# Optimization experiments

Measured on AMD Instinct MI355X. Metric: run time of the kernel, lower is better.

Reference implementation:

```python
import jax, jax.numpy as jnp
import numpy as np

D_MODEL = 1024
N_HEADS = 16
D_HEAD = D_MODEL // N_HEADS
B, S = 2, 2048


def setup_inputs() -> dict:
    key = jax.random.key(0)
    ks = jax.random.split(key, 8)
    scale = 1.0 / np.sqrt(D_MODEL)
    return {
        "x": jax.random.normal(ks[0], (B, S, D_MODEL), dtype=jnp.float32),
        "Wq": jax.random.normal(ks[1], (D_MODEL, D_MODEL), dtype=jnp.float32) * scale,
        "bq": jnp.zeros((D_MODEL,), dtype=jnp.float32),
        "Wk": jax.random.normal(ks[2], (D_MODEL, D_MODEL), dtype=jnp.float32) * scale,
        "bk": jnp.zeros((D_MODEL,), dtype=jnp.float32),
        "Wv": jax.random.normal(ks[3], (D_MODEL, D_MODEL), dtype=jnp.float32) * scale,
        "bv": jnp.zeros((D_MODEL,), dtype=jnp.float32),
        "Wo": jax.random.normal(ks[4], (D_MODEL, D_MODEL), dtype=jnp.float32) * scale,
    }


def reference(x, Wq, bq, Wk, bk, Wv, bv, Wo):
    Bsz, Slen, D = x.shape
    # projections -> [B, H, S, Dh]
    def split_heads(t):
        return t.reshape(Bsz, Slen, N_HEADS, D_HEAD).transpose(0, 2, 1, 3)
    q = split_heads(x @ Wq + bq)
    k = split_heads(x @ Wk + bk)
    v = split_heads(x @ Wv + bv)
    scale = jnp.sqrt(jnp.float32(D_HEAD))
    scores = jnp.einsum('bhsd,bhtd->bhst', q, k) / scale  # [B,H,S,S]
    causal_mask = jnp.tril(jnp.ones((Slen, Slen), dtype=jnp.bool_))
    scores = jnp.where(causal_mask, scores, jnp.finfo(scores.dtype).min)
    attn = jax.nn.softmax(scores, axis=-1)
    # deterministic=True path: dropout is identity
    out = jnp.einsum('bhst,bhtd->bhsd', attn, v)
    out = out.transpose(0, 2, 1, 3).reshape(Bsz, Slen, D)
    return out @ Wo
```

## Files before the change

### kernel.cpp

```cpp
#include <hip/hip_runtime.h>
#include <hip/hip_bf16.h>

#define BATCH   2
#define SEQ     2048
#define DMODEL  1024
#define NHEADS  16
#define DHEAD   64
#define MROWS   (BATCH*SEQ)

typedef float  f32x4  __attribute__((ext_vector_type(4)));
typedef short  s16x4  __attribute__((ext_vector_type(4)));
typedef short  s16x8  __attribute__((ext_vector_type(8)));
typedef __bf16 bf16x8 __attribute__((ext_vector_type(8)));

__device__ __forceinline__ short f2bf(float f) {
  union { float f; unsigned u; } v; v.f = f;
  return (short)((v.u + 0x7fffu + ((v.u >> 16) & 1u)) >> 16);
}

__global__ void convert_x(const float* __restrict__ x, short* __restrict__ xb) {
  int i = (blockIdx.x * 256 + threadIdx.x) * 4;
  float4 v = *(const float4*)(x + i);
  s16x4 o = { f2bf(v.x), f2bf(v.y), f2bf(v.z), f2bf(v.w) };
  *(s16x4*)(xb + i) = o;
}

__global__ void transpose_w(const float* __restrict__ Wq, const float* __restrict__ Wk,
                            const float* __restrict__ Wv, const float* __restrict__ Wo,
                            short* __restrict__ WtQKV, short* __restrict__ WtO) {
  __shared__ float t[32][33];
  const float* W; short* Wt;
  int z = blockIdx.z;
  if      (z == 0) { W = Wq; Wt = WtQKV; }
  else if (z == 1) { W = Wk; Wt = WtQKV + (1u << 20); }
  else if (z == 2) { W = Wv; Wt = WtQKV + (2u << 20); }
  else             { W = Wo; Wt = WtO; }
  int n0 = blockIdx.x * 32, k0 = blockIdx.y * 32;
  int tx = threadIdx.x, ty = threadIdx.y;
  #pragma unroll
  for (int i = 0; i < 32; i += 8) t[ty + i][tx] = W[(k0 + ty + i) * DMODEL + n0 + tx];
  __syncthreads();
  #pragma unroll
  for (int i = 0; i < 32; i += 8) Wt[(n0 + ty + i) * DMODEL + k0 + tx] = f2bf(t[tx][ty + i]);
}

template<int MT, int NT, int EPI>
__global__ __launch_bounds__(256) void gemm_bf16(
    const short* __restrict__ A, const short* __restrict__ Bt,
    const float* __restrict__ bq, const float* __restrict__ bk, const float* __restrict__ bv,
    short* __restrict__ qb, short* __restrict__ kb, short* __restrict__ vt,
    float* __restrict__ out)
{
  constexpr int K = DMODEL, BK = 32;
  constexpr int WM = MT / 2, WN = NT / 2;
  constexpr int TM = WM / 16, TN = WN / 16;
  constexpr int CA = MT * BK / 512;
  constexpr int CB = NT * BK / 512;
  constexpr int TP = 136;
  constexpr int SME = (EPI == 0) ? 128 * TP : (MT * BK + NT * BK);
  __shared__ short smem[SME];
  short* la = smem;
  short* lb = smem + MT * BK;
  const int tid = threadIdx.x;
  const int wave = tid >> 6, lane = tid & 63;
  const int quad = lane >> 4, l16 = lane & 15;
  const int wr = wave >> 1, wc = wave & 1;
  const int m0 = blockIdx.y * MT, n0 = blockIdx.x * NT;
  const int arow = lane >> 2, acol = (lane & 3) * 8;

  f32x4 acc[TM][TN] = {};

  for (int k0 = 0; k0 < K; k0 += BK) {
    for (int c = wave; c < CA; c += 4) {
      const short* gp = A + (m0 + c * 16 + arow) * K + k0 + acol;
      __builtin_amdgcn_global_load_lds((__attribute__((address_space(1))) void*)gp,
                                       (__attribute__((address_space(3))) void*)(la + c * 512),
                                       16, 0, 0);
    }
    for (int c = wave; c < CB; c += 4) {
      const short* gp = Bt + (n0 + c * 16 + arow) * K + k0 + acol;
      __builtin_amdgcn_global_load_lds((__attribute__((address_space(1))) void*)gp,
                                       (__attribute__((address_space(3))) void*)(lb + c * 512),
                                       16, 0, 0);
    }
    __syncthreads();
    bf16x8 af[TM], bfr[TN];
    #pragma unroll
    for (int i = 0; i < TM; ++i)
      af[i] = *(const bf16x8*)&la[(wr * WM + i * 16 + l16) * BK + quad * 8];
    #pragma unroll
    for (int j = 0; j < TN; ++j)
      bfr[j] = *(const bf16x8*)&lb[(wc * WN + j * 16 + l16) * BK + quad * 8];
    #pragma unroll
    for (int i = 0; i < TM; ++i)
      #pragma unroll
      for (int j = 0; j < TN; ++j)
        acc[i][j] = __builtin_amdgcn_mfma_f32_16x16x32_bf16(af[i], bfr[j], acc[i][j], 0, 0, 0);
    __syncthreads();
  }

  if constexpr (EPI == 0) {
    const bool isV = (n0 >= 2 * DMODEL);
    const float* bias; int nbase; float scl;
    if (n0 < DMODEL)          { bias = bq; nbase = 0;          scl = 0.125f * 1.44269504089f; }
    else if (n0 < 2 * DMODEL) { bias = bk; nbase = DMODEL;     scl = 1.f; }
    else                      { bias = bv; nbase = 2 * DMODEL; scl = 1.f; }
    #pragma unroll
    for (int j = 0; j < TN; ++j) {
      int coll = wc * WN + j * 16 + l16;
      float bias_v = bias[n0 - nbase + coll];
      #pragma unroll
      for (int i = 0; i < TM; ++i) {
        int rowl = wr * WM + i * 16 + quad * 4;
        #pragma unroll
        for (int r = 0; r < 4; ++r) {
          short v = f2bf((acc[i][j][r] + bias_v) * scl);
          if (isV) smem[coll * TP + rowl + r] = v;
          else     smem[(rowl + r) * TP + coll] = v;
        }
      }
    }
    __syncthreads();
    const int b = m0 >> 11, s0 = m0 & (SEQ - 1);
    const int rseg = tid & 15, rrow = tid >> 4;
    if (!isV) {
      short* dst = (n0 < DMODEL) ? qb : kb;
      #pragma unroll
      for (int it = 0; it < 8; ++it) {
        int row = it * 16 + rrow;
        int colg = (n0 - nbase) + rseg * 8;
        int h = colg >> 6, d = colg & 63;
        s16x8 v = *(const s16x8*)&smem[row * TP + rseg * 8];
        *(s16x8*)(dst + ((b * NHEADS + h) * SEQ + s0 + row) * DHEAD + d) = v;
      }
    } else {
      #pragma unroll
      for (int it = 0; it < 8; ++it) {
        int drow = it * 16 + rrow;
        int colg = (n0 - nbase) + drow;
        int h = colg >> 6, d = colg & 63;
        s16x8 v = *(const s16x8*)&smem[drow * TP + rseg * 8];
        *(s16x8*)(vt + ((b * NHEADS + h) * DHEAD + d) * SEQ + s0 + rseg * 8) = v;
      }
    }
  } else {
    #pragma unroll
    for (int i = 0; i < TM; ++i)
      #pragma unroll
      for (int r = 0; r < 4; ++r) {
        int mrow = m0 + wr * WM + i * 16 + quad * 4 + r;
        #pragma unroll
        for (int j = 0; j < TN; ++j)
          out[mrow * DMODEL + n0 + wc * WN + j * 16 + l16] = acc[i][j][r];
      }
    (void)bq; (void)bk; (void)bv; (void)qb; (void)kb; (void)vt;
  }
}


__global__ __launch_bounds__(128, 2) void attn_k(
    const short* __restrict__ qbp, const short* __restrict__ kbp,
    const short* __restrict__ vtb, short* __restrict__ ob)
{
  __shared__ short kls[2][4096];
  __shared__ short vls[2][4096];
  const int tid = threadIdx.x, wave = tid >> 6, lane = tid & 63;
  const int quad = lane >> 4, l16 = lane & 15;
  const int bh = blockIdx.x >> 5;
  const int qg = blockIdx.x & 31;
  const int qt = qg * 2 + wave;
  const int ma = qt * 16;
  const int mb = (127 - qt) * 16;
  const int nch = (127 - qg * 2) / 4 + 1;
  const short* Q  = qbp + bh * SEQ * DHEAD;
  const short* Kp = kbp + bh * SEQ * DHEAD;
  const short* Vt = vtb + bh * DHEAD * SEQ;

  bf16x8 qa0 = *(const bf16x8*)&Q[(ma + l16) * DHEAD + quad * 8];
  bf16x8 qa1 = *(const bf16x8*)&Q[(ma + l16) * DHEAD + 32 + quad * 8];
  bf16x8 qb0 = *(const bf16x8*)&Q[(mb + l16) * DHEAD + quad * 8];
  bf16x8 qb1 = *(const bf16x8*)&Q[(mb + l16) * DHEAD + 32 + quad * 8];

  float lA = 0.f, lB = 0.f;
  f32x4 oA[4] = {}, oB[4] = {};

  const int vdl = lane >> 3, vsl = lane & 7;

  auto stage = [&](int buf, int t0) {
    #pragma unroll
    for (int j = 0; j < 4; ++j) {
      int g = j * 2 + wave;
      const short* gp = Kp + (t0 + lane) * DHEAD + g * 8;
      __builtin_amdgcn_global_load_lds((__attribute__((address_space(1))) void*)gp,
                                       (__attribute__((address_space(3))) void*)&kls[buf][g * 512],
                                       16, 0, 0);
    }
    #pragma unroll
    for (int j = 0; j < 4; ++j) {
      int gd = j * 2 + wave;
      const short* gp = Vt + (gd * 8 + vdl) * SEQ + t0 + ((vsl ^ vdl) * 8);
      __builtin_amdgcn_global_load_lds((__attribute__((address_space(1))) void*)gp,
                                       (__attribute__((address_space(3))) void*)&vls[buf][gd * 512],
                                       16, 0, 0);
    }
  };

  auto frag = [&](const bf16x8 kf[4][2], const s16x4 vf[4][4], int t0, int mF,
                  bf16x8 f0, bf16x8 f1, float& lF, f32x4 oF[4]) {
    const int nlive = (mF - t0) / 16 + 1;
    #pragma unroll
    for (int t = 0; t < 4; ++t) {
      if (t < nlive) {
        f32x4 a = {};
        a = __builtin_amdgcn_mfma_f32_16x16x32_bf16(kf[t][0], f0, a, 0, 0, 0);
        a = __builtin_amdgcn_mfma_f32_16x16x32_bf16(kf[t][1], f1, a, 0, 0, 0);
        if (t0 + t * 16 == mF) {
          #pragma unroll
          for (int r = 0; r < 4; ++r)
            if (quad * 4 + r > l16) a[r] = -1e30f;
        }
        f32x4 p;
        #pragma unroll
        for (int r = 0; r < 4; ++r) p[r] = __builtin_amdgcn_exp2f(a[r]);
        lF += (p[0] + p[1]) + (p[2] + p[3]);
        __hip_bfloat162 c01 = __float22bfloat162_rn(float2{p[0], p[1]});
        __hip_bfloat162 c23 = __float22bfloat162_rn(float2{p[2], p[3]});
        union { unsigned u[2]; s16x4 s; } pu;
        pu.u[0] = *(unsigned*)&c01; pu.u[1] = *(unsigned*)&c23;
        #pragma unroll
        for (int dt = 0; dt < 4; ++dt)
          oF[dt] = __builtin_amdgcn_mfma_f32_16x16x16bf16_1k(pu.s, vf[t][dt], oF[dt], 0, 0, 0);
      }
    }
  };

  stage(0, 0);
  for (int c = 0; c < nch; ++c) {
    __syncthreads();
    if (c + 1 < nch) stage((c + 1) & 1, (c + 1) * 64);
    const int t0 = c * 64;
    const int buf = c & 1;
    bf16x8 kf[4][2];
    #pragma unroll
    for (int t = 0; t < 4; ++t)
      #pragma unroll
      for (int h = 0; h < 2; ++h)
        kf[t][h] = *(const bf16x8*)&kls[buf][((h * 4 + quad) * 64 + t * 16 + l16) * 8];
    s16x4 vf[4][4];
    #pragma unroll
    for (int t = 0; t < 4; ++t) {
      int gsw = ((t * 2 + (quad >> 1)) ^ (l16 & 7));
      #pragma unroll
      for (int dt = 0; dt < 4; ++dt)
        vf[t][dt] = *(const s16x4*)&vls[buf][((dt * 16 + l16) * 8 + gsw) * 8 + (quad & 1) * 4];
    }
    if (t0 <= mb) frag(kf, vf, t0, mb, qb0, qb1, lB, oB);
    if (t0 <= ma) frag(kf, vf, t0, ma, qa0, qa1, lA, oA);
  }

  lA += __shfl_xor(lA, 16, 64); lA += __shfl_xor(lA, 32, 64);
  lB += __shfl_xor(lB, 16, 64); lB += __shfl_xor(lB, 32, 64);
  const int b = bh >> 4, h = bh & 15;
  #pragma unroll
  for (int r = 0; r < 4; ++r) {
    float liA = 1.0f / __shfl(lA, quad * 4 + r, 64);
    float liB = 1.0f / __shfl(lB, quad * 4 + r, 64);
    int sA = ma + quad * 4 + r, sB = mb + quad * 4 + r;
    #pragma unroll
    for (int dt = 0; dt < 4; ++dt) {
      ob[(b * SEQ + sA) * DMODEL + h * DHEAD + dt * 16 + l16] = f2bf(oA[dt][r] * liA);
      ob[(b * SEQ + sB) * DMODEL + h * DHEAD + dt * 16 + l16] = f2bf(oB[dt][r] * liB);
    }
  }
}

extern "C" void kernel_launch(void* const* d_in, const int* in_sizes, int n_in,
                              void* d_out, int out_size, void* d_ws, size_t ws_size,
                              hipStream_t stream) {
  const float* x  = (const float*)d_in[0];
  const float* Wq = (const float*)d_in[1];
  const float* bq = (const float*)d_in[2];
  const float* Wk = (const float*)d_in[3];
  const float* bk = (const float*)d_in[4];
  const float* Wv = (const float*)d_in[5];
  const float* bv = (const float*)d_in[6];
  const float* Wo = (const float*)d_in[7];
  float* out = (float*)d_out;

  char* ws = (char*)d_ws;
  short* xb  = (short*)(ws);
  short* wtq = (short*)(ws + (8u  << 20));
  short* wto = (short*)(ws + (14u << 20));
  short* qb  = (short*)(ws + (16u << 20));
  short* kb  = (short*)(ws + (24u << 20));
  short* vt  = (short*)(ws + (32u << 20));
  short* ob  = (short*)(ws + (40u << 20));

  convert_x<<<MROWS * DMODEL / 1024, 256, 0, stream>>>(x, xb);
  transpose_w<<<dim3(32, 32, 4), dim3(32, 8), 0, stream>>>(Wq, Wk, Wv, Wo, wtq, wto);

  gemm_bf16<128, 128, 0><<<dim3(3 * DMODEL / 128, MROWS / 128), 256, 0, stream>>>(
      xb, wtq, bq, bk, bv, qb, kb, vt, nullptr);

  attn_k<<<BATCH * NHEADS * 32, 128, 0, stream>>>(qb, kb, vt, ob);

  gemm_bf16<64, 128, 1><<<dim3(DMODEL / 128, MROWS / 64), 256, 0, stream>>>(
      ob, wto, nullptr, nullptr, nullptr, nullptr, nullptr, nullptr, out);
}
```

Before: 207.0 us.

## Split attention KV range across two blocks and merge partial outputs

The attention kernel now uses 4 waves per block, each block covering 4 query tiles paired causally. Each block processes only alternating 64-key chunks (even or odd by a half index), so the KV loop is split across two blocks. Unnormalized partial outputs and row sums go to workspace, and a new merge kernel adds them and normalizes. This aims to cut per-block serial loop length and balance work, at the cost of extra partial-output traffic, an extra launch, and bf16 rounding of the partials before the merge.

```diff
diff --git a/kernel.cpp b/kernel.cpp
--- a/kernel.cpp
+++ b/kernel.cpp
@@ -7,6 +7,7 @@
 #define NHEADS  16
 #define DHEAD   64
 #define MROWS   (BATCH*SEQ)
+#define NBH     (BATCH*NHEADS)
 
 typedef float  f32x4  __attribute__((ext_vector_type(4)));
 typedef short  s16x4  __attribute__((ext_vector_type(4)));
@@ -16,6 +17,10 @@
 __device__ __forceinline__ short f2bf(float f) {
   union { float f; unsigned u; } v; v.f = f;
   return (short)((v.u + 0x7fffu + ((v.u >> 16) & 1u)) >> 16);
+}
+__device__ __forceinline__ float bf2f(short s) {
+  union { unsigned u; float f; } v; v.u = ((unsigned)(unsigned short)s) << 16;
+  return v.f;
 }
 
 __global__ void convert_x(const float* __restrict__ x, short* __restrict__ xb) {
@@ -158,20 +163,21 @@
 }
 
 
-__global__ __launch_bounds__(128, 2) void attn_k(
+__global__ __launch_bounds__(256, 2) void attn_k(
     const short* __restrict__ qbp, const short* __restrict__ kbp,
-    const short* __restrict__ vtb, short* __restrict__ ob)
+    const short* __restrict__ vtb, short* __restrict__ oP, float* __restrict__ lP)
 {
   __shared__ short kls[2][4096];
   __shared__ short vls[2][4096];
   const int tid = threadIdx.x, wave = tid >> 6, lane = tid & 63;
   const int quad = lane >> 4, l16 = lane & 15;
-  const int bh = blockIdx.x >> 5;
-  const int qg = blockIdx.x & 31;
-  const int qt = qg * 2 + wave;
+  const int half = blockIdx.x & 1;
+  const int bh = (blockIdx.x >> 1) & 31;
+  const int qg = blockIdx.x >> 6;
+  const int qt = qg * 4 + wave;
   const int ma = qt * 16;
   const int mb = (127 - qt) * 16;
-  const int nch = (127 - qg * 2) / 4 + 1;
+  const int nch = (127 - qg * 4) / 4 + 1;
   const short* Q  = qbp + bh * SEQ * DHEAD;
   const short* Kp = kbp + bh * SEQ * DHEAD;
   const short* Vt = vtb + bh * DHEAD * SEQ;
@@ -188,16 +194,16 @@
 
   auto stage = [&](int buf, int t0) {
     #pragma unroll
-    for (int j = 0; j < 4; ++j) {
-      int g = j * 2 + wave;
+    for (int j = 0; j < 2; ++j) {
+      int g = j * 4 + wave;
       const short* gp = Kp + (t0 + lane) * DHEAD + g * 8;
       __builtin_amdgcn_global_load_lds((__attribute__((address_space(1))) void*)gp,
                                        (__attribute__((address_space(3))) void*)&kls[buf][g * 512],
                                        16, 0, 0);
     }
     #pragma unroll
-    for (int j = 0; j < 4; ++j) {
-      int gd = j * 2 + wave;
+    for (int j = 0; j < 2; ++j) {
+      int gd = j * 4 + wave;
       const short* gp = Vt + (gd * 8 + vdl) * SEQ + t0 + ((vsl ^ vdl) * 8);
       __builtin_amdgcn_global_load_lds((__attribute__((address_space(1))) void*)gp,
                                        (__attribute__((address_space(3))) void*)&vls[buf][gd * 512],
@@ -234,12 +240,12 @@
     }
   };
 
-  stage(0, 0);
-  for (int c = 0; c < nch; ++c) {
+  stage(0, half * 64);
+  for (int c = half; c < nch; c += 2) {
     __syncthreads();
-    if (c + 1 < nch) stage((c + 1) & 1, (c + 1) * 64);
+    if (c + 2 < nch) stage(((c >> 1) + 1) & 1, (c + 2) * 64);
     const int t0 = c * 64;
-    const int buf = c & 1;
+    const int buf = (c >> 1) & 1;
     bf16x8 kf[4][2];
     #pragma unroll
     for (int t = 0; t < 4; ++t)
@@ -260,18 +266,32 @@
 
   lA += __shfl_xor(lA, 16, 64); lA += __shfl_xor(lA, 32, 64);
   lB += __shfl_xor(lB, 16, 64); lB += __shfl_xor(lB, 32, 64);
-  const int b = bh >> 4, h = bh & 15;
+  float* lD = lP + (half * NBH + bh) * SEQ;
+  if (quad == 0) { lD[ma + l16] = lA; lD[mb + l16] = lB; }
+  short* oD = oP + ((half * NBH + bh) * SEQ) * DHEAD;
   #pragma unroll
   for (int r = 0; r < 4; ++r) {
-    float liA = 1.0f / __shfl(lA, quad * 4 + r, 64);
-    float liB = 1.0f / __shfl(lB, quad * 4 + r, 64);
     int sA = ma + quad * 4 + r, sB = mb + quad * 4 + r;
     #pragma unroll
     for (int dt = 0; dt < 4; ++dt) {
-      ob[(b * SEQ + sA) * DMODEL + h * DHEAD + dt * 16 + l16] = f2bf(oA[dt][r] * liA);
-      ob[(b * SEQ + sB) * DMODEL + h * DHEAD + dt * 16 + l16] = f2bf(oB[dt][r] * liB);
+      oD[sA * DHEAD + dt * 16 + l16] = f2bf(oA[dt][r]);
+      oD[sB * DHEAD + dt * 16 + l16] = f2bf(oB[dt][r]);
     }
   }
+}
+
+__global__ void attn_merge(const short* __restrict__ oP, const float* __restrict__ lP,
+                           short* __restrict__ ob) {
+  int idx = blockIdx.x * 256 + threadIdx.x;
+  int d8 = idx & 7, s = (idx >> 3) & (SEQ - 1), bh = idx >> 14;
+  s16x8 e = *(const s16x8*)&oP[((0   + bh) * SEQ + s) * DHEAD + d8 * 8];
+  s16x8 o = *(const s16x8*)&oP[((NBH + bh) * SEQ + s) * DHEAD + d8 * 8];
+  float linv = 1.0f / (lP[bh * SEQ + s] + lP[(NBH + bh) * SEQ + s]);
+  s16x8 r;
+  #pragma unroll
+  for (int k = 0; k < 8; ++k) r[k] = f2bf((bf2f(e[k]) + bf2f(o[k])) * linv);
+  int b = bh >> 4, h = bh & 15;
+  *(s16x8*)&ob[(b * SEQ + s) * DMODEL + h * DHEAD + d8 * 8] = r;
 }
 
 extern "C" void kernel_launch(void* const* d_in, const int* in_sizes, int n_in,
@@ -290,11 +310,13 @@
   char* ws = (char*)d_ws;
   short* xb  = (short*)(ws);
   short* wtq = (short*)(ws + (8u  << 20));
-  short* wto = (short*)(ws + (14u << 20));
+  short* oP  = (short*)(ws);
   short* qb  = (short*)(ws + (16u << 20));
   short* kb  = (short*)(ws + (24u << 20));
   short* vt  = (short*)(ws + (32u << 20));
   short* ob  = (short*)(ws + (40u << 20));
+  short* wto = (short*)(ws + (48u << 20));
+  float* lP  = (float*)(ws + (50u << 20));
 
   convert_x<<<MROWS * DMODEL / 1024, 256, 0, stream>>>(x, xb);
   transpose_w<<<dim3(32, 32, 4), dim3(32, 8), 0, stream>>>(Wq, Wk, Wv, Wo, wtq, wto);
@@ -302,7 +324,8 @@
   gemm_bf16<128, 128, 0><<<dim3(3 * DMODEL / 128, MROWS / 128), 256, 0, stream>>>(
       xb, wtq, bq, bk, bv, qb, kb, vt, nullptr);
 
-  attn_k<<<BATCH * NHEADS * 32, 128, 0, stream>>>(qb, kb, vt, ob);
+  attn_k<<<NBH * 16 * 2, 256, 0, stream>>>(qb, kb, vt, oP, lP);
+  attn_merge<<<NBH * SEQ * 8 / 256, 256, 0, stream>>>(oP, lP, ob);
 
   gemm_bf16<64, 128, 1><<<dim3(DMODEL / 128, MROWS / 64), 256, 0, stream>>>(
       ob, wto, nullptr, nullptr, nullptr, nullptr, nullptr, nullptr, out);
```

New measurement: 198.6 us. 1.04x faster.
